# Optimization experiments

Measured on AMD Instinct MI355X. Metric: run time of the kernel, lower is better.

Reference implementation:

```python
import jax, jax.numpy as jnp
import numpy as np


def setup_inputs() -> dict:
    key = jax.random.key(0)
    k1, k2, k3, k4 = jax.random.split(key, 4)
    B, n, f, k = 32768, 512, 30, 40
    X = jax.random.normal(k1, (B, n), dtype=jnp.float32)
    w1 = jax.random.normal(k2, (n, 1), dtype=jnp.float32) * 0.01
    b = jnp.zeros((1,), dtype=jnp.float32)
    v = jax.random.normal(k3, (n, f, k), dtype=jnp.float32) * 0.01
    feature2field = jax.random.randint(k4, (n,), 0, f, dtype=jnp.int32)
    return {"X": X, "w1": w1, "b": b, "v": v, "feature2field": feature2field}


def reference(X, w1, b, v, feature2field):
    # linear terms: [B]
    linear = (X @ w1).reshape(-1) + b[0]
    n = v.shape[0]
    # A[i, j] = v[i, feature2field[j]]  -> [n, n, k]
    A = v[:, feature2field, :]
    # pair coefficient C[i, j] = sum_k v[i, field[j], k] * v[j, field[i], k]
    C = jnp.einsum('ijk,jik->ij', A, A)
    # strict upper triangle matches the i<j loop in the original
    Cm = C * jnp.triu(jnp.ones((n, n), dtype=C.dtype), k=1)
    # interaction[b] = sum_{i<j} C[i,j] * X[b,i] * X[b,j]
    inter = jnp.einsum('bi,ij,bj->b', X, Cm, X)
    logits = linear + inter
    return jax.nn.sigmoid(logits)
```

## Files before the change

### kernel.cpp

```cpp
#include <hip/hip_runtime.h>
#include <hip/hip_bf16.h>
#include <math.h>


#define N_FEAT 512
#define FK 1200
#define KDIM 40
#define B_ROWS 32768
#define BM 64
#define NSTEP 16

typedef __attribute__((ext_vector_type(8))) short short8;
typedef __attribute__((ext_vector_type(16))) float f32x16;

__device__ __forceinline__ unsigned short bf16_rne(float f) {
    union { float f; unsigned int u; } c; c.f = f;
    unsigned int u = c.u;
    u += 0x7fffu + ((u >> 16) & 1u);
    return (unsigned short)(u >> 16);
}

__device__ __forceinline__ float bf16_to_f(unsigned short h) {
    union { unsigned int u; float f; } c;
    c.u = ((unsigned int)h) << 16;
    return c.f;
}

__global__ __launch_bounds__(256) void build_wpk(const float* __restrict__ v,
                                                 const int* __restrict__ f2f,
                                                 unsigned short* __restrict__ Wpk) {
    __shared__ float a_lds[FK];
    __shared__ float c_lds[256 * 44];

    const int i   = blockIdx.y;
    const int j0  = blockIdx.x * 256;
    const int tid = threadIdx.x;
    const int fi  = f2f[i];

    for (int q = tid; q < FK; q += 256) a_lds[q] = v[(size_t)i * FK + q];
    for (int q = tid; q < 2560; q += 256) {
        const int jl = q / 10, c4 = q % 10;
        *(float4*)&c_lds[jl * 44 + c4 * 4] =
            *(const float4*)&v[(size_t)(j0 + jl) * FK + fi * KDIM + c4 * 4];
    }
    __syncthreads();

    const int j  = j0 + tid;
    const int fj = f2f[j];
    const float4* a = (const float4*)&a_lds[fj * KDIM];
    const float4* c = (const float4*)&c_lds[tid * 44];
    float acc = 0.f;
#pragma unroll
    for (int q = 0; q < KDIM / 4; ++q) {
        float4 av = a[q], cv = c[q];
        acc = fmaf(av.x, cv.x, acc);
        acc = fmaf(av.y, cv.y, acc);
        acc = fmaf(av.z, cv.z, acc);
        acc = fmaf(av.w, cv.w, acc);
    }
    const unsigned short val = (i == j) ? (unsigned short)0 : bf16_rne(0.5f * acc);
    Wpk[((size_t)(j >> 3) * 512 + i) * 8 + (j & 7)] = val;
}

__global__ __launch_bounds__(512, 2) void ffm_fused(const float* __restrict__ X,
                                                    const unsigned short* __restrict__ Wpk,
                                                    const float* __restrict__ w1,
                                                    const float* __restrict__ bvec,
                                                    float* __restrict__ out) {
    __shared__ __align__(16) unsigned short As[BM * N_FEAT];
    __shared__ float part[8 * BM];

    const int tid  = threadIdx.x;
    const int lane = tid & 63;
    const int wave = tid >> 6;
    const int half = lane >> 5;
    const int l31  = lane & 31;

    const size_t row0 = (size_t)blockIdx.x * BM;

    const unsigned short* wp = Wpk + ((size_t)half * 512 + wave * 64 + l31) * 8;

    {
        const float4* X4 = (const float4*)(X + row0 * N_FEAT);
#pragma unroll
        for (int u = 0; u < 8; ++u) {
            const int g  = u * 512 + tid;
            const int r  = g >> 6;
            const int kc = g & 63;
            float4 f0 = X4[r * 128 + kc * 2];
            float4 f1 = X4[r * 128 + kc * 2 + 1];
            union { unsigned short us[8]; short8 v; } pk;
            pk.us[0] = bf16_rne(f0.x);
            pk.us[1] = bf16_rne(f0.y);
            pk.us[2] = bf16_rne(f0.z);
            pk.us[3] = bf16_rne(f0.w);
            pk.us[4] = bf16_rne(f1.x);
            pk.us[5] = bf16_rne(f1.y);
            pk.us[6] = bf16_rne(f1.z);
            pk.us[7] = bf16_rne(f1.w);
            *(short8*)(As + ((size_t)kc * 64 + (r ^ (kc & 7))) * 8) = pk.v;
        }
    }
    asm volatile("s_waitcnt lgkmcnt(0)" ::: "memory");
    __builtin_amdgcn_s_barrier();

    f32x16 acc[2][2];
#pragma unroll
    for (int mi = 0; mi < 2; ++mi)
#pragma unroll
        for (int ci = 0; ci < 2; ++ci)
#pragma unroll
            for (int r = 0; r < 16; ++r) acc[mi][ci][r] = 0.f;

    short8 fb[2][2][2];
#pragma unroll
    for (int si = 0; si < 2; ++si)
#pragma unroll
        for (int ci = 0; ci < 2; ++ci)
            fb[0][si][ci] = *(const short8*)(wp + ((size_t)(si * 2) * 512 + ci * 32) * 8);

#pragma unroll
    for (int t = 0; t < NSTEP; ++t) {
        const int cur = t & 1;
        const int nxt = cur ^ 1;

        if (t + 1 < NSTEP) {
#pragma unroll
            for (int si = 0; si < 2; ++si)
#pragma unroll
                for (int ci = 0; ci < 2; ++ci)
                    fb[nxt][si][ci] = *(const short8*)(wp +
                        ((size_t)((t + 1) * 4 + si * 2) * 512 + ci * 32) * 8);
        }

        short8 a[2][2];
#pragma unroll
        for (int si = 0; si < 2; ++si) {
            const int kcg = t * 4 + si * 2 + half;
            const int ksw = kcg & 7;
#pragma unroll
            for (int mi = 0; mi < 2; ++mi)
                a[si][mi] = *(const short8*)(As +
                    ((size_t)kcg * 64 + ((mi * 32 + l31) ^ ksw)) * 8);
        }

        __builtin_amdgcn_s_setprio(1);
#pragma unroll
        for (int si = 0; si < 2; ++si)
#pragma unroll
            for (int mi = 0; mi < 2; ++mi)
#pragma unroll
                for (int ci = 0; ci < 2; ++ci)
                    acc[mi][ci] = __builtin_amdgcn_mfma_f32_32x32x16_bf16(
                        a[si][mi], fb[cur][si][ci], acc[mi][ci], 0, 0, 0);
        __builtin_amdgcn_s_setprio(0);
    }

    float w1v[2];
#pragma unroll
    for (int ci = 0; ci < 2; ++ci) w1v[ci] = w1[wave * 64 + ci * 32 + l31];
    const float bias = bvec[0];

    float rs[2][16];
#pragma unroll
    for (int mi = 0; mi < 2; ++mi) {
#pragma unroll
        for (int reg = 0; reg < 16; ++reg) {
            const int row = mi * 32 + (reg & 3) + 8 * (reg >> 2) + 4 * half;
            float s = 0.f;
#pragma unroll
            for (int ci = 0; ci < 2; ++ci) {
                const int gc = wave * 64 + ci * 32 + l31;
                const int kc = gc >> 3;
                const float xf = bf16_to_f(As[((size_t)kc * 64 + (row ^ (kc & 7))) * 8 + (gc & 7)]);
                s = fmaf(xf, acc[mi][ci][reg] + w1v[ci], s);
            }
            rs[mi][reg] = s;
        }
    }

#pragma unroll
    for (int mi = 0; mi < 2; ++mi)
#pragma unroll
        for (int reg = 0; reg < 16; ++reg) {
            float r = rs[mi][reg];
#pragma unroll
            for (int off = 1; off < 32; off <<= 1)
                r += __shfl_xor(r, off, 32);
            rs[mi][reg] = r;
        }
    if (l31 == 0) {
#pragma unroll
        for (int mi = 0; mi < 2; ++mi)
#pragma unroll
            for (int reg = 0; reg < 16; ++reg) {
                const int row = mi * 32 + (reg & 3) + 8 * (reg >> 2) + 4 * half;
                part[wave * 64 + row] = rs[mi][reg];
            }
    }
    __syncthreads();

    if (tid < BM) {
        float tsum = bias;
#pragma unroll
        for (int w = 0; w < 8; ++w) tsum += part[w * 64 + tid];
        out[row0 + tid] = 1.0f / (1.0f + expf(-tsum));
    }
}

extern "C" void kernel_launch(void* const* d_in, const int* in_sizes, int n_in,
                              void* d_out, int out_size, void* d_ws, size_t ws_size,
                              hipStream_t stream) {
    const float* X   = (const float*)d_in[0];
    const float* w1  = (const float*)d_in[1];
    const float* b   = (const float*)d_in[2];
    const float* v   = (const float*)d_in[3];
    const int*   f2f = (const int*)d_in[4];
    float* out = (float*)d_out;

    unsigned short* Wpk = (unsigned short*)d_ws;

    build_wpk<<<dim3(2, N_FEAT), 256, 0, stream>>>(v, f2f, Wpk);
    ffm_fused<<<B_ROWS / BM, 512, 0, stream>>>(X, Wpk, w1, b, out);
}
```

Measured before the change: 128.2 us.

## Enlarge row tile to 128 with 2x4 wave grid and rotated K order

Doubles the batch tile to 128 rows and arranges the 8 waves as 2 (rows) x 4 (columns), so each wave computes a 64x128 output tile and every W fragment loaded from global memory feeds twice as many MFMAs. The K loop start is rotated per block to spread W reads across blocks, and both A (LDS) and B (global) fragments are now double-buffered, with B prefetched two steps ahead. The cost is 128 KB of LDS per block and more accumulator registers, which limits occupancy to one block per CU and halves the block count.

```diff
diff --git a/kernel.cpp b/kernel.cpp
--- a/kernel.cpp
+++ b/kernel.cpp
@@ -7,7 +7,7 @@
 #define FK 1200
 #define KDIM 40
 #define B_ROWS 32768
-#define BM 64
+#define BM 128
 #define NSTEP 16
 
 typedef __attribute__((ext_vector_type(8))) short short8;
@@ -62,28 +62,31 @@
     Wpk[((size_t)(j >> 3) * 512 + i) * 8 + (j & 7)] = val;
 }
 
-__global__ __launch_bounds__(512, 2) void ffm_fused(const float* __restrict__ X,
+__global__ __launch_bounds__(512, 1) void ffm_fused(const float* __restrict__ X,
                                                     const unsigned short* __restrict__ Wpk,
                                                     const float* __restrict__ w1,
                                                     const float* __restrict__ bvec,
                                                     float* __restrict__ out) {
     __shared__ __align__(16) unsigned short As[BM * N_FEAT];
-    __shared__ float part[8 * BM];
+    __shared__ float part[4 * BM];
 
     const int tid  = threadIdx.x;
     const int lane = tid & 63;
     const int wave = tid >> 6;
     const int half = lane >> 5;
     const int l31  = lane & 31;
+    const int wm   = wave & 1;
+    const int wn   = wave >> 1;
 
     const size_t row0 = (size_t)blockIdx.x * BM;
-
-    const unsigned short* wp = Wpk + ((size_t)half * 512 + wave * 64 + l31) * 8;
+    const int rot = blockIdx.x & (NSTEP - 1);
+
+    const unsigned short* wp = Wpk + ((size_t)half * 512 + wn * 128 + l31) * 8;
 
     {
         const float4* X4 = (const float4*)(X + row0 * N_FEAT);
 #pragma unroll
-        for (int u = 0; u < 8; ++u) {
+        for (int u = 0; u < 16; ++u) {
             const int g  = u * 512 + tid;
             const int r  = g >> 6;
             const int kc = g & 63;
@@ -98,26 +101,45 @@
             pk.us[5] = bf16_rne(f1.y);
             pk.us[6] = bf16_rne(f1.z);
             pk.us[7] = bf16_rne(f1.w);
-            *(short8*)(As + ((size_t)kc * 64 + (r ^ (kc & 7))) * 8) = pk.v;
+            *(short8*)(As + ((size_t)kc * BM + (r ^ (kc & 7))) * 8) = pk.v;
         }
     }
     asm volatile("s_waitcnt lgkmcnt(0)" ::: "memory");
     __builtin_amdgcn_s_barrier();
 
-    f32x16 acc[2][2];
+    f32x16 acc[2][4];
 #pragma unroll
     for (int mi = 0; mi < 2; ++mi)
 #pragma unroll
-        for (int ci = 0; ci < 2; ++ci)
+        for (int ci = 0; ci < 4; ++ci)
 #pragma unroll
             for (int r = 0; r < 16; ++r) acc[mi][ci][r] = 0.f;
 
-    short8 fb[2][2][2];
-#pragma unroll
-    for (int si = 0; si < 2; ++si)
-#pragma unroll
-        for (int ci = 0; ci < 2; ++ci)
-            fb[0][si][ci] = *(const short8*)(wp + ((size_t)(si * 2) * 512 + ci * 32) * 8);
+    short8 fb[2][2][4];
+    short8 fa[2][2][2];
+
+    {
+        const int tr0 = rot;
+        const int tr1 = (rot + 1) & (NSTEP - 1);
+#pragma unroll
+        for (int si = 0; si < 2; ++si)
+#pragma unroll
+            for (int ci = 0; ci < 4; ++ci) {
+                fb[0][si][ci] = *(const short8*)(wp +
+                    ((size_t)(tr0 * 4 + si * 2) * 512 + ci * 32) * 8);
+                fb[1][si][ci] = *(const short8*)(wp +
+                    ((size_t)(tr1 * 4 + si * 2) * 512 + ci * 32) * 8);
+            }
+#pragma unroll
+        for (int si = 0; si < 2; ++si) {
+            const int kcg = tr0 * 4 + si * 2 + half;
+            const int ksw = kcg & 7;
+#pragma unroll
+            for (int mi = 0; mi < 2; ++mi)
+                fa[0][si][mi] = *(const short8*)(As +
+                    ((size_t)kcg * BM + ((wm * 64 + mi * 32 + l31) ^ ksw)) * 8);
+        }
+    }
 
 #pragma unroll
     for (int t = 0; t < NSTEP; ++t) {
@@ -125,40 +147,43 @@
         const int nxt = cur ^ 1;
 
         if (t + 1 < NSTEP) {
+            const int trn = (t + 1 + rot) & (NSTEP - 1);
+#pragma unroll
+            for (int si = 0; si < 2; ++si) {
+                const int kcg = trn * 4 + si * 2 + half;
+                const int ksw = kcg & 7;
+#pragma unroll
+                for (int mi = 0; mi < 2; ++mi)
+                    fa[nxt][si][mi] = *(const short8*)(As +
+                        ((size_t)kcg * BM + ((wm * 64 + mi * 32 + l31) ^ ksw)) * 8);
+            }
+        }
+
+        __builtin_amdgcn_s_setprio(1);
+#pragma unroll
+        for (int si = 0; si < 2; ++si)
+#pragma unroll
+            for (int mi = 0; mi < 2; ++mi)
+#pragma unroll
+                for (int ci = 0; ci < 4; ++ci)
+                    acc[mi][ci] = __builtin_amdgcn_mfma_f32_32x32x16_bf16(
+                        fa[cur][si][mi], fb[cur][si][ci], acc[mi][ci], 0, 0, 0);
+        __builtin_amdgcn_s_setprio(0);
+
+        if (t + 2 < NSTEP) {
+            const int trn2 = (t + 2 + rot) & (NSTEP - 1);
 #pragma unroll
             for (int si = 0; si < 2; ++si)
 #pragma unroll
-                for (int ci = 0; ci < 2; ++ci)
-                    fb[nxt][si][ci] = *(const short8*)(wp +
-                        ((size_t)((t + 1) * 4 + si * 2) * 512 + ci * 32) * 8);
-        }
-
-        short8 a[2][2];
-#pragma unroll
-        for (int si = 0; si < 2; ++si) {
-            const int kcg = t * 4 + si * 2 + half;
-            const int ksw = kcg & 7;
-#pragma unroll
-            for (int mi = 0; mi < 2; ++mi)
-                a[si][mi] = *(const short8*)(As +
-                    ((size_t)kcg * 64 + ((mi * 32 + l31) ^ ksw)) * 8);
-        }
-
-        __builtin_amdgcn_s_setprio(1);
-#pragma unroll
-        for (int si = 0; si < 2; ++si)
-#pragma unroll
-            for (int mi = 0; mi < 2; ++mi)
-#pragma unroll
-                for (int ci = 0; ci < 2; ++ci)
-                    acc[mi][ci] = __builtin_amdgcn_mfma_f32_32x32x16_bf16(
-                        a[si][mi], fb[cur][si][ci], acc[mi][ci], 0, 0, 0);
-        __builtin_amdgcn_s_setprio(0);
-    }
-
-    float w1v[2];
-#pragma unroll
-    for (int ci = 0; ci < 2; ++ci) w1v[ci] = w1[wave * 64 + ci * 32 + l31];
+                for (int ci = 0; ci < 4; ++ci)
+                    fb[cur][si][ci] = *(const short8*)(wp +
+                        ((size_t)(trn2 * 4 + si * 2) * 512 + ci * 32) * 8);
+        }
+    }
+
+    float w1v[4];
+#pragma unroll
+    for (int ci = 0; ci < 4; ++ci) w1v[ci] = w1[wn * 128 + ci * 32 + l31];
     const float bias = bvec[0];
 
     float rs[2][16];
@@ -166,13 +191,13 @@
     for (int mi = 0; mi < 2; ++mi) {
 #pragma unroll
         for (int reg = 0; reg < 16; ++reg) {
-            const int row = mi * 32 + (reg & 3) + 8 * (reg >> 2) + 4 * half;
+            const int row = wm * 64 + mi * 32 + (reg & 3) + 8 * (reg >> 2) + 4 * half;
             float s = 0.f;
 #pragma unroll
-            for (int ci = 0; ci < 2; ++ci) {
-                const int gc = wave * 64 + ci * 32 + l31;
+            for (int ci = 0; ci < 4; ++ci) {
+                const int gc = wn * 128 + ci * 32 + l31;
                 const int kc = gc >> 3;
-                const float xf = bf16_to_f(As[((size_t)kc * 64 + (row ^ (kc & 7))) * 8 + (gc & 7)]);
+                const float xf = bf16_to_f(As[((size_t)kc * BM + (row ^ (kc & 7))) * 8 + (gc & 7)]);
                 s = fmaf(xf, acc[mi][ci][reg] + w1v[ci], s);
             }
             rs[mi][reg] = s;
@@ -194,8 +219,8 @@
         for (int mi = 0; mi < 2; ++mi)
 #pragma unroll
             for (int reg = 0; reg < 16; ++reg) {
-                const int row = mi * 32 + (reg & 3) + 8 * (reg >> 2) + 4 * half;
-                part[wave * 64 + row] = rs[mi][reg];
+                const int row = wm * 64 + mi * 32 + (reg & 3) + 8 * (reg >> 2) + 4 * half;
+                part[wn * BM + row] = rs[mi][reg];
             }
     }
     __syncthreads();
@@ -203,7 +228,7 @@
     if (tid < BM) {
         float tsum = bias;
 #pragma unroll
-        for (int w = 0; w < 8; ++w) tsum += part[w * 64 + tid];
+        for (int q = 0; q < 4; ++q) tsum += part[q * BM + tid];
         out[row0 + tid] = 1.0f / (1.0f + expf(-tsum));
     }
 }
```

Result: no change. 129.9 us (+1.3%).
